# Performance work log

Measured on AMD Instinct MI355X. Metric: run time of the kernel, lower is better.

Reference implementation:

```python
import jax, jax.numpy as jnp
import numpy as np

N = 50000   # nodes
E = 600000  # edges
IN = 512    # in_channels
H = 128     # hidden_channels
B = 64      # graphs in batch
L = 4       # GatedGraphConv layers
VIEWS = [[0, 9, 10], [1, 2, 3], [4, 5, 6], [7, 8, 11, 12]]  # syntactic/sequential/semantic/discourse


def layer_norm(x, w, b, eps=1e-5):
    mu = x.mean(-1, keepdims=True)
    var = ((x - mu) ** 2).mean(-1, keepdims=True)
    return (x - mu) / jnp.sqrt(var + eps) * w + b


def setup_inputs() -> dict:
    key = jax.random.key(0)
    ks = jax.random.split(key, 32)
    p = lambda k, shape: (jax.random.normal(k, shape, jnp.float32) * 0.02)
    inp = {
        'x': jax.random.normal(ks[0], (N, IN), jnp.float32),
        'edge_index': jax.random.randint(ks[1], (2, E), 0, N, dtype=jnp.int32),
        'edge_type': jax.random.randint(ks[2], (E,), 0, 13, dtype=jnp.int32),
        'batch': jnp.sort(jax.random.randint(ks[3], (N,), 0, B, dtype=jnp.int32)),
        # input projection (Linear + LayerNorm)
        'proj_w': p(ks[4], (IN, H)), 'proj_b': p(ks[5], (H,)),
        'ln0_w': jnp.ones((H,), jnp.float32), 'ln0_b': jnp.zeros((H,), jnp.float32),
        # per-view GatedGraphConv: weight [views, layers, H, H] + GRUCell params [views, 3H, H]
        'ggnn_w': p(ks[6], (4, L, H, H)),
        'gru_wih': p(ks[7], (4, 3 * H, H)), 'gru_whh': p(ks[8], (4, 3 * H, H)),
        'gru_bih': p(ks[9], (4, 3 * H)), 'gru_bhh': p(ks[10], (4, 3 * H)),
        # per-view LayerNorm
        'vln_w': jnp.ones((4, H), jnp.float32), 'vln_b': jnp.zeros((4, H), jnp.float32),
        # attention fusion
        'q_w': p(ks[11], (H, H)), 'q_b': p(ks[12], (H,)),
        'k_w': p(ks[13], (H, H)), 'k_b': p(ks[14], (H,)),
        # classifier MLP: 2H -> H -> H//2 -> 1
        'c1_w': p(ks[15], (2 * H, H)), 'c1_b': p(ks[16], (H,)),
        'c2_w': p(ks[17], (H, H // 2)), 'c2_b': p(ks[18], (H // 2,)),
        'c3_w': p(ks[19], (H // 2, 1)), 'c3_b': p(ks[20], (1,)),
    }
    return inp


def reference(x, edge_index, edge_type, batch, proj_w, proj_b, ln0_w, ln0_b,
              ggnn_w, gru_wih, gru_whh, gru_bih, gru_bhh, vln_w, vln_b,
              q_w, q_b, k_w, k_b, c1_w, c1_b, c2_w, c2_b, c3_w, c3_b):
    # input projection: Linear -> LayerNorm -> GELU (dropout = identity in eval)
    h0 = jax.nn.gelu(layer_norm(x @ proj_w + proj_b, ln0_w, ln0_b), approximate=False)
    src, dst = edge_index[0], edge_index[1]
    views = []
    for v in range(4):
        emask = jnp.zeros((E,), bool)
        for t in VIEWS[v]:
            emask = emask | (edge_type == t)
        em = emask.astype(h0.dtype)[:, None]  # [E,1] edge-type view mask
        h = h0
        for i in range(L):
            m = h @ ggnn_w[v, i]                                   # [N,H]
            agg = jax.ops.segment_sum(m[src] * em, dst, num_segments=N)  # masked scatter-add
            # GRUCell(input=agg, hidden=h), torch gate order r,z,n
            gi = agg @ gru_wih[v].T + gru_bih[v]
            gh = h @ gru_whh[v].T + gru_bhh[v]
            ir, iz, inn = jnp.split(gi, 3, -1)
            hr, hz, hn = jnp.split(gh, 3, -1)
            r = jax.nn.sigmoid(ir + hr)
            z = jax.nn.sigmoid(iz + hz)
            n = jnp.tanh(inn + r * hn)
            h = (1.0 - z) * n + z * h
        views.append(layer_norm(h, vln_w[v], vln_b[v]) + h0)  # residual ViewEncoder
    hs = jnp.stack(views, 1)  # [N,4,H]
    # node-conditioned attention fusion
    q = jnp.tanh(h0 @ q_w + q_b)
    keys = hs @ k_w + k_b
    attn = jax.nn.softmax(jnp.einsum('nh,nvh->nv', q, keys) * (H ** -0.5), axis=-1)
    fused = jnp.einsum('nvh,nv->nh', hs, attn)
    # global mean + max pooling per graph
    cnt = jax.ops.segment_sum(jnp.ones((N,), fused.dtype), batch, num_segments=B)
    x_mean = jax.ops.segment_sum(fused, batch, num_segments=B) / jnp.maximum(cnt, 1.0)[:, None]
    x_max = jax.ops.segment_max(fused, batch, num_segments=B)
    g = jnp.concatenate([x_mean, x_max], -1)  # [B,2H]
    h1 = jax.nn.relu(g @ c1_w + c1_b)
    h2 = jax.nn.relu(h1 @ c2_w + c2_b)
    return h2 @ c3_w + c3_b  # [B,1] logits
```

## Files before the change

### kernel.cpp

```cpp
#include <hip/hip_runtime.h>
#include <math.h>


typedef __attribute__((ext_vector_type(8))) short short8;
typedef __attribute__((ext_vector_type(4))) float floatx4;

__device__ __forceinline__ unsigned short f2bf_rtn(float x) {
    unsigned u = __float_as_uint(x);
    return (unsigned short)((u + 0x7FFFu + ((u >> 16) & 1u)) >> 16);
}
__device__ __forceinline__ float bf2f(unsigned short h) {
    return __uint_as_float((unsigned)h << 16);
}
__device__ __forceinline__ float fsig(float x) {
    return __builtin_amdgcn_rcpf(1.0f + __expf(-x));
}
__device__ __forceinline__ float ftanh(float x) {
    return 1.0f - 2.0f * __builtin_amdgcn_rcpf(__expf(2.0f * x) + 1.0f);
}

__device__ __forceinline__ int view_of(int t) {
    return (t >= 1 && t <= 3) ? 1 : (t >= 4 && t <= 6) ? 2
         : ((t == 7) || (t == 8) || (t >= 11)) ? 3 : 0;
}

template <bool BT, int EPI>
__global__ __launch_bounds__(256, 2) void gemm_k(
    const float* __restrict__ A, const float* __restrict__ Bm,
    const float* __restrict__ bias, float* __restrict__ C,
    int N, int M, int K, long sA, long sB, long sC)
{
    __shared__ float As[32][132];
    __shared__ float Bs[32][132];
    A  += (long)blockIdx.z * sA;
    Bm += (long)blockIdx.z * sB;
    C  += (long)blockIdx.z * sC;
    const int r0 = blockIdx.x * 128;
    const int c0 = blockIdx.y * 128;
    const int tid = threadIdx.x;
    const int tx = tid & 15;
    const int ty = tid >> 4;

    float acc[8][8];
#pragma unroll
    for (int i = 0; i < 8; i++)
#pragma unroll
        for (int j = 0; j < 8; j++) acc[i][j] = 0.0f;

    for (int k0 = 0; k0 < K; k0 += 32) {
        {
            int arow = tid >> 3;
            int akq  = (tid & 7) << 2;
#pragma unroll
            for (int hh = 0; hh < 4; hh++) {
                int r  = arow + hh * 32;
                int gr = r0 + r;
                float4 av = make_float4(0.f, 0.f, 0.f, 0.f);
                if (gr < N) av = *(const float4*)(A + (long)gr * K + k0 + akq);
                As[akq + 0][r] = av.x; As[akq + 1][r] = av.y;
                As[akq + 2][r] = av.z; As[akq + 3][r] = av.w;
            }
        }
        if (BT) {
            int brow = tid >> 3;
            int bkq  = (tid & 7) << 2;
#pragma unroll
            for (int hh = 0; hh < 4; hh++) {
                int r = brow + hh * 32;
                float4 bv = *(const float4*)(Bm + (long)(c0 + r) * K + k0 + bkq);
                Bs[bkq + 0][r] = bv.x; Bs[bkq + 1][r] = bv.y;
                Bs[bkq + 2][r] = bv.z; Bs[bkq + 3][r] = bv.w;
            }
        } else {
            int kk0 = tid >> 5;
            int bmq = (tid & 31) << 2;
#pragma unroll
            for (int hh = 0; hh < 4; hh++) {
                int kk = kk0 + hh * 8;
                float4 bv = *(const float4*)(Bm + (long)(k0 + kk) * M + c0 + bmq);
                *(float4*)&Bs[kk][bmq] = bv;
            }
        }
        __syncthreads();
#pragma unroll
        for (int k = 0; k < 32; k++) {
            float4 a0 = *(const float4*)&As[k][ty << 2];
            float4 a1 = *(const float4*)&As[k][64 + (ty << 2)];
            float4 b0 = *(const float4*)&Bs[k][tx << 2];
            float4 b1 = *(const float4*)&Bs[k][64 + (tx << 2)];
            float av[8] = {a0.x, a0.y, a0.z, a0.w, a1.x, a1.y, a1.z, a1.w};
            float bv[8] = {b0.x, b0.y, b0.z, b0.w, b1.x, b1.y, b1.z, b1.w};
#pragma unroll
            for (int i = 0; i < 8; i++)
#pragma unroll
                for (int j = 0; j < 8; j++) acc[i][j] += av[i] * bv[j];
        }
        __syncthreads();
    }

    float bb[8] = {0, 0, 0, 0, 0, 0, 0, 0};
    if (bias) {
        float4 b0 = *(const float4*)(bias + c0 + (tx << 2));
        float4 b1 = *(const float4*)(bias + c0 + 64 + (tx << 2));
        bb[0] = b0.x; bb[1] = b0.y; bb[2] = b0.z; bb[3] = b0.w;
        bb[4] = b1.x; bb[5] = b1.y; bb[6] = b1.z; bb[7] = b1.w;
    }
#pragma unroll
    for (int i = 0; i < 8; i++) {
        int r = (i < 4) ? (r0 + (ty << 2) + i) : (r0 + 64 + (ty << 2) + i - 4);
        if (r < N) {
            float v[8];
#pragma unroll
            for (int j = 0; j < 8; j++) {
                v[j] = acc[i][j] + bb[j];
                if (EPI == 1) v[j] = tanhf(v[j]);
            }
            *(float4*)(C + (long)r * M + c0 + (tx << 2)) = make_float4(v[0], v[1], v[2], v[3]);
            *(float4*)(C + (long)r * M + c0 + 64 + (tx << 2)) = make_float4(v[4], v[5], v[6], v[7]);
        }
    }
}

__global__ __launch_bounds__(256) void build_p_k(
    const float* __restrict__ gwih, const float* __restrict__ gwhh,
    const float* __restrict__ gbih, const float* __restrict__ gbhh,
    float* __restrict__ pih, float* __restrict__ phh, float* __restrict__ bp)
{
    int idx = blockIdx.x * 256 + threadIdx.x;
    if (idx < 16 * 65536) {
        int z = idx >> 16, rem = idx & 65535;
        int k = rem >> 9, mcol = rem & 511;
        int ch = mcol >> 2, g = mcol & 3;
        int v = z >> 2;
        const float* Wih = gwih + (long)v * 384 * 128;
        float val = 0.0f;
        if (g == 0) val = Wih[ch * 128 + k];
        else if (g == 1) val = Wih[(128 + ch) * 128 + k];
        else if (g == 2) val = Wih[(256 + ch) * 128 + k];
        pih[idx] = val;
    }
    if (idx < 4 * 65536) {
        int v = idx >> 16, rem = idx & 65535;
        int k = rem >> 9, mcol = rem & 511;
        int ch = mcol >> 2, g = mcol & 3;
        const float* Whh = gwhh + (long)v * 384 * 128;
        float val = 0.0f;
        if (g == 0) val = Whh[ch * 128 + k];
        else if (g == 1) val = Whh[(128 + ch) * 128 + k];
        else if (g == 3) val = Whh[(256 + ch) * 128 + k];
        phh[idx] = val;
    }
    if (idx < 4 * 512) {
        int v = idx >> 9, mcol = idx & 511;
        int ch = mcol >> 2, g = mcol & 3;
        float val;
        if (g == 0) val = gbih[v * 384 + ch] + gbhh[v * 384 + ch];
        else if (g == 1) val = gbih[v * 384 + 128 + ch] + gbhh[v * 384 + 128 + ch];
        else if (g == 2) val = gbih[v * 384 + 256 + ch];
        else val = gbhh[v * 384 + 256 + ch];
        bp[idx] = val;
    }
}

__global__ __launch_bounds__(256) void pack_b_k(
    const float* __restrict__ wcomb, const float* __restrict__ phh,
    short* __restrict__ Bp)
{
    int idx = blockIdx.x * 256 + threadIdx.x;
    if (idx >= 16 * 256 * 512) return;
    int z = idx >> 17, rem = idx & 131071;
    int k = rem >> 9, col = rem & 511;
    int g  = col & 3;
    int q  = (col >> 2) & 3;
    int tn = (col >> 4) & 7;
    int ch = ((col >> 7) << 5) + (q << 3) + tn;
    int mcol = (ch << 2) + g;
    float val = (k < 128) ? wcomb[(long)z * 65536 + k * 512 + mcol]
                          : phh[(long)(z >> 2) * 65536 + (k - 128) * 512 + mcol];
    long dst = ((long)(z * 8 + (k >> 5)) * 512 + col) * 32 + ((k >> 3) & 3) * 8 + (k & 7);
    Bp[dst] = (short)f2bf_rtn(val);
}

template <bool BT>
__global__ __launch_bounds__(256) void pack_w_k(
    const float* __restrict__ W, short* __restrict__ bhi, short* __restrict__ blo, int K)
{
    int idx = blockIdx.x * 256 + threadIdx.x;
    if (idx >= K * 128) return;
    int k = idx >> 7, col = idx & 127;
    float v = BT ? W[col * K + k] : W[k * 128 + col];
    unsigned short h = f2bf_rtn(v);
    float fh = __uint_as_float((unsigned)h << 16);
    long dst = ((long)(k >> 5) * 128 + col) * 32 + ((k >> 3) & 3) * 8 + (k & 7);
    bhi[dst] = (short)h;
    blo[dst] = (short)f2bf_rtn(v - fh);
}

template <int EPI>
__global__ __launch_bounds__(256, 4) void gemm_mfma_k(
    const float* __restrict__ A, const short* __restrict__ Bhi,
    const short* __restrict__ Blo, const float* __restrict__ bias,
    float* __restrict__ C, int N, int K)
{
    __shared__ __align__(16) short Ahi[64 * 40];
    __shared__ __align__(16) short Alo[64 * 40];
    const int r0 = blockIdx.x * 64;
    const int tid = threadIdx.x;
    const int l = tid & 63, w = tid >> 6;
    const int wrow = w * 16;
    const int m = l & 15, q = l >> 4;

    floatx4 acc[8];
#pragma unroll
    for (int b = 0; b < 8; b++) acc[b] = (floatx4)0.0f;

    const int arow = tid >> 2;
    const int fcol = (tid & 3) * 8;
    const int gr = r0 + arow;
    const int nks = K >> 5;

    for (int ks = 0; ks < nks; ks++) {
        float xv[8];
        if (gr < N) {
            float4 x0 = *(const float4*)(A + (long)gr * K + ks * 32 + fcol);
            float4 x1 = *(const float4*)(A + (long)gr * K + ks * 32 + fcol + 4);
            xv[0] = x0.x; xv[1] = x0.y; xv[2] = x0.z; xv[3] = x0.w;
            xv[4] = x1.x; xv[5] = x1.y; xv[6] = x1.z; xv[7] = x1.w;
        } else {
#pragma unroll
            for (int u = 0; u < 8; u++) xv[u] = 0.0f;
        }
        short8 vhi, vlo;
#pragma unroll
        for (int u = 0; u < 8; u++) {
            unsigned short hb = f2bf_rtn(xv[u]);
            float fh = __uint_as_float((unsigned)hb << 16);
            vhi[u] = (short)hb;
            vlo[u] = (short)f2bf_rtn(xv[u] - fh);
        }
        *(short8*)&Ahi[arow * 40 + fcol] = vhi;
        *(short8*)&Alo[arow * 40 + fcol] = vlo;
        __syncthreads();
        short8 ah = *(short8*)&Ahi[(wrow + m) * 40 + q * 8];
        short8 al = *(short8*)&Alo[(wrow + m) * 40 + q * 8];
#pragma unroll
        for (int tn = 0; tn < 8; tn++) {
            int col = tn * 16 + m;
            short8 bh = *(const short8*)(Bhi + ((long)ks * 128 + col) * 32 + q * 8);
            short8 bl = *(const short8*)(Blo + ((long)ks * 128 + col) * 32 + q * 8);
            acc[tn] = __builtin_amdgcn_mfma_f32_16x16x32_bf16(ah, bh, acc[tn], 0, 0, 0);
            acc[tn] = __builtin_amdgcn_mfma_f32_16x16x32_bf16(al, bh, acc[tn], 0, 0, 0);
            acc[tn] = __builtin_amdgcn_mfma_f32_16x16x32_bf16(ah, bl, acc[tn], 0, 0, 0);
        }
        __syncthreads();
    }

#pragma unroll
    for (int tn = 0; tn < 8; tn++) {
        int col = tn * 16 + m;
        float bb = bias ? bias[col] : 0.0f;
#pragma unroll
        for (int reg = 0; reg < 4; reg++) {
            int row = r0 + wrow + q * 4 + reg;
            if (row < N) {
                float v = acc[tn][reg] + bb;
                if (EPI == 1) v = ftanh(v);
                C[(long)row * 128 + col] = v;
            }
        }
    }
}

__global__ __launch_bounds__(256, 3) void gemm_gru_mfma_k(
    const short* __restrict__ hb, const float* __restrict__ hpf,
    const short* __restrict__ Bp, const float* __restrict__ bp,
    float* __restrict__ hf, short* __restrict__ hbn,
    const int* __restrict__ off, const int* __restrict__ esrc,
    int N, long sV, long sHb, long sHp)
{
    __shared__ __align__(16) short As[8 * 64 * 40];
    const int xb = blockIdx.x;
    const int x = (xb & 7) | ((xb >> 4) << 3);
    const int yb = (xb >> 3) & 1;
    if (x * 64 >= N) return;
    const int z = blockIdx.z;
    const short* hbz = hb + (long)z * sHb;
    hpf += (long)z * sHp;
    Bp  += (long)z * 524288;
    bp  += (long)z * 512;
    hf  += (long)z * sV;
    hbn += (long)z * sV;
    const int r0  = x * 64;
    const int c0b = yb * 256;
    const int tid = threadIdx.x;
    const int l = tid & 63, w = tid >> 6;
    const int wrow = (w & 1) * 32, wcol = (w >> 1) * 128;
    const int m = l & 15, q = l >> 4;

    floatx4 acc[2][8];
#pragma unroll
    for (int a = 0; a < 2; a++)
#pragma unroll
        for (int b = 0; b < 8; b++) acc[a][b] = (floatx4)0.0f;

    const int arow = tid >> 2;
    const int fcol = (tid & 3) * 8;
    const int gr = r0 + arow;

    {
        const int cg = tid & 3;
        float accS[32];
#pragma unroll
        for (int u = 0; u < 32; u++) accS[u] = 0.0f;
        if (gr < N) {
            const int idx = z * N + gr;
            const int beg = off[idx], end = off[idx + 1];
            for (int j = beg; j < end; j++) {
                const short* sp = hb + (long)esrc[j] * 128 + (cg << 5);
                short8 v0 = *(const short8*)(sp);
                short8 v1 = *(const short8*)(sp + 8);
                short8 v2 = *(const short8*)(sp + 16);
                short8 v3 = *(const short8*)(sp + 24);
#pragma unroll
                for (int u = 0; u < 8; u++) {
                    accS[u]      += bf2f((unsigned short)v0[u]);
                    accS[8 + u]  += bf2f((unsigned short)v1[u]);
                    accS[16 + u] += bf2f((unsigned short)v2[u]);
                    accS[24 + u] += bf2f((unsigned short)v3[u]);
                }
            }
        }
#pragma unroll
        for (int ub = 0; ub < 4; ub++) {
            short8 o;
#pragma unroll
            for (int u = 0; u < 8; u++) o[u] = (short)f2bf_rtn(accS[ub * 8 + u]);
            *(short8*)&As[cg * 2560 + arow * 40 + ub * 8] = o;
        }
    }

#pragma unroll
    for (int ks2 = 0; ks2 < 4; ks2++) {
        short8 av = (short8)0;
        if (gr < N) av = *(const short8*)(hbz + (long)gr * 128 + ks2 * 32 + fcol);
        *(short8*)&As[(4 + ks2) * 2560 + arow * 40 + fcol] = av;
    }
    __syncthreads();

#pragma unroll
    for (int ks = 0; ks < 8; ks++) {
        short8 bfr[8];
#pragma unroll
        for (int tn = 0; tn < 8; tn++) {
            int col = c0b + wcol + tn * 16 + m;
            bfr[tn] = *(const short8*)(Bp + ((long)ks * 512 + col) * 32 + q * 8);
        }
        short8 a0 = *(short8*)&As[ks * 2560 + (wrow + m) * 40 + q * 8];
        short8 a1 = *(short8*)&As[ks * 2560 + (wrow + 16 + m) * 40 + q * 8];
#pragma unroll
        for (int tn = 0; tn < 8; tn++) {
            acc[0][tn] = __builtin_amdgcn_mfma_f32_16x16x32_bf16(bfr[tn], a0, acc[0][tn], 0, 0, 0);
            acc[1][tn] = __builtin_amdgcn_mfma_f32_16x16x32_bf16(bfr[tn], a1, acc[1][tn], 0, 0, 0);
        }
    }

    const int chq = ((c0b + wcol) >> 2) + q * 8;
#pragma unroll
    for (int a = 0; a < 2; a++) {
        const int row = r0 + wrow + a * 16 + m;
        if (row < N) {
            float4 hp0 = *(const float4*)(hpf + (long)row * 128 + chq);
            float4 hp1 = *(const float4*)(hpf + (long)row * 128 + chq + 4);
            float hpv[8] = {hp0.x, hp0.y, hp0.z, hp0.w, hp1.x, hp1.y, hp1.z, hp1.w};
            float hnv[8];
            short8 hb8;
#pragma unroll
            for (int tn = 0; tn < 8; tn++) {
                float4 bv = *(const float4*)(bp + (chq + tn) * 4);
                floatx4 A = acc[a][tn];
                float rr = fsig(A[0] + bv.x);
                float zz = fsig(A[1] + bv.y);
                float nn = ftanh(A[2] + bv.z + rr * (A[3] + bv.w));
                hnv[tn] = (1.0f - zz) * nn + zz * hpv[tn];
                hb8[tn] = (short)f2bf_rtn(hnv[tn]);
            }
            *(float4*)(hf + (long)row * 128 + chq) =
                make_float4(hnv[0], hnv[1], hnv[2], hnv[3]);
            *(float4*)(hf + (long)row * 128 + chq + 4) =
                make_float4(hnv[4], hnv[5], hnv[6], hnv[7]);
            *(short8*)(hbn + (long)row * 128 + chq) = hb8;
        }
    }
}

__global__ __launch_bounds__(256) void ln_gelu_k(
    float* __restrict__ h0, short* __restrict__ h0b,
    const float* __restrict__ w, const float* __restrict__ b, int N)
{
    long t = (long)blockIdx.x * 256 + threadIdx.x;
    int n = (int)(t >> 5), lane = (int)(t & 31);
    if (n >= N) return;
    float* p = h0 + (long)n * 128 + lane * 4;
    float4 x = *(float4*)p;
    float s = x.x + x.y + x.z + x.w;
#pragma unroll
    for (int off = 16; off >= 1; off >>= 1) s += __shfl_xor(s, off);
    float mu = s * (1.0f / 128.0f);
    float4 d = make_float4(x.x - mu, x.y - mu, x.z - mu, x.w - mu);
    float ss = d.x * d.x + d.y * d.y + d.z * d.z + d.w * d.w;
#pragma unroll
    for (int off = 16; off >= 1; off >>= 1) ss += __shfl_xor(ss, off);
    float inv = 1.0f / sqrtf(ss * (1.0f / 128.0f) + 1e-5f);
    float4 wv = *(const float4*)(w + lane * 4);
    float4 bv = *(const float4*)(b + lane * 4);
    float y[4] = {d.x * inv * wv.x + bv.x, d.y * inv * wv.y + bv.y,
                  d.z * inv * wv.z + bv.z, d.w * inv * wv.w + bv.w};
#pragma unroll
    for (int i = 0; i < 4; i++)
        y[i] = 0.5f * y[i] * (1.0f + erff(y[i] * 0.70710678118654752f));
    *(float4*)p = make_float4(y[0], y[1], y[2], y[3]);
    ushort4 hb;
    hb.x = f2bf_rtn(y[0]); hb.y = f2bf_rtn(y[1]);
    hb.z = f2bf_rtn(y[2]); hb.w = f2bf_rtn(y[3]);
    *(ushort4*)(h0b + (long)n * 128 + lane * 4) = hb;
}

__global__ __launch_bounds__(256) void count_k(
    const int* __restrict__ dst, const int* __restrict__ et,
    int* __restrict__ cnt, int E, int N)
{
    int e = blockIdx.x * 256 + threadIdx.x;
    if (e >= E) return;
    int v = view_of(et[e]);
    atomicAdd(&cnt[v * N + dst[e]], 1);
}

__global__ __launch_bounds__(256) void scan1_k(
    const int* __restrict__ cnt, int* __restrict__ off, int* __restrict__ bsum, int n)
{
    __shared__ int sm[256];
    int base = blockIdx.x * 1024;
    int tid = threadIdx.x;
    int v[4]; int s = 0;
#pragma unroll
    for (int i = 0; i < 4; i++) {
        int idx = base + tid * 4 + i;
        v[i] = (idx < n) ? cnt[idx] : 0; s += v[i];
    }
    sm[tid] = s; __syncthreads();
    for (int o = 1; o < 256; o <<= 1) {
        int t2 = (tid >= o) ? sm[tid - o] : 0;
        __syncthreads(); sm[tid] += t2; __syncthreads();
    }
    int run = sm[tid] - s;
    if (tid == 255) bsum[blockIdx.x] = sm[255];
#pragma unroll
    for (int i = 0; i < 4; i++) {
        int idx = base + tid * 4 + i;
        if (idx < n) off[idx] = run;
        run += v[i];
    }
}

__global__ __launch_bounds__(256) void scan2_k(int* __restrict__ bsum, int nb)
{
    __shared__ int sm[256];
    int tid = threadIdx.x;
    int v = (tid < nb) ? bsum[tid] : 0;
    sm[tid] = v; __syncthreads();
    for (int o = 1; o < 256; o <<= 1) {
        int t2 = (tid >= o) ? sm[tid - o] : 0;
        __syncthreads(); sm[tid] += t2; __syncthreads();
    }
    if (tid < nb) bsum[tid] = sm[tid] - v;
}

__global__ __launch_bounds__(256) void scan3_k(
    int* __restrict__ off, int* __restrict__ cursor,
    const int* __restrict__ bsum, int n, int total)
{
    int i = blockIdx.x * 256 + threadIdx.x;
    if (i < n) {
        int o = off[i] + bsum[i >> 10];
        off[i] = o; cursor[i] = o;
    }
    if (i == 0) off[n] = total;
}

__global__ __launch_bounds__(256) void fill_k(
    const int* __restrict__ src, const int* __restrict__ dst,
    const int* __restrict__ et, int* __restrict__ cursor,
    int* __restrict__ esrc, int* __restrict__ esrc0, int E, int N)
{
    int e = blockIdx.x * 256 + threadIdx.x;
    if (e >= E) return;
    int v = view_of(et[e]);
    int b = v * N + dst[e];
    int pos = atomicAdd(&cursor[b], 1);
    esrc[pos] = v * N + src[e];
    esrc0[pos] = src[e];
}

__global__ __launch_bounds__(256) void vln_res_k(
    float* __restrict__ h, const float* __restrict__ h0,
    const float* __restrict__ w, const float* __restrict__ b, int N)
{
    int v = blockIdx.z;
    long t = (long)blockIdx.x * 256 + threadIdx.x;
    int n = (int)(t >> 5), lane = (int)(t & 31);
    if (n >= N) return;
    float* hp = h + ((long)v * N + n) * 128 + lane * 4;
    float4 x = *(float4*)hp;
    float s = x.x + x.y + x.z + x.w;
#pragma unroll
    for (int off = 16; off >= 1; off >>= 1) s += __shfl_xor(s, off);
    float mu = s * (1.0f / 128.0f);
    float4 d = make_float4(x.x - mu, x.y - mu, x.z - mu, x.w - mu);
    float ss = d.x * d.x + d.y * d.y + d.z * d.z + d.w * d.w;
#pragma unroll
    for (int off = 16; off >= 1; off >>= 1) ss += __shfl_xor(ss, off);
    float inv = 1.0f / sqrtf(ss * (1.0f / 128.0f) + 1e-5f);
    float4 wv = *(const float4*)(w + v * 128 + lane * 4);
    float4 bv = *(const float4*)(b + v * 128 + lane * 4);
    float4 hv = *(const float4*)(h0 + (long)n * 128 + lane * 4);
    float4 r;
    r.x = d.x * inv * wv.x + bv.x + hv.x;
    r.y = d.y * inv * wv.y + bv.y + hv.y;
    r.z = d.z * inv * wv.z + bv.z + hv.z;
    r.w = d.w * inv * wv.w + bv.w + hv.w;
    *(float4*)hp = r;
}

__global__ __launch_bounds__(256) void fusion_k(
    const float* __restrict__ hs, const float* __restrict__ q,
    const float* __restrict__ u, const float* __restrict__ kb,
    float* __restrict__ fused, int N)
{
    long t = (long)blockIdx.x * 256 + threadIdx.x;
    int n = (int)(t >> 5), lane = (int)(t & 31);
    if (n >= N) return;
    long NH = (long)N * 128;
    float4 qv = *(const float4*)(q + (long)n * 128 + lane * 4);
    float4 kv = *(const float4*)(kb + lane * 4);
    float4 uv = *(const float4*)(u + (long)n * 128 + lane * 4);
    float part = qv.x * kv.x + qv.y * kv.y + qv.z * kv.z + qv.w * kv.w;
    float4 hv[4];
    float lg[4];
#pragma unroll
    for (int v = 0; v < 4; v++) {
        hv[v] = *(const float4*)(hs + v * NH + (long)n * 128 + lane * 4);
        lg[v] = hv[v].x * uv.x + hv[v].y * uv.y + hv[v].z * uv.z + hv[v].w * uv.w;
    }
#pragma unroll
    for (int off = 16; off >= 1; off >>= 1) {
        part += __shfl_xor(part, off);
#pragma unroll
        for (int v = 0; v < 4; v++) lg[v] += __shfl_xor(lg[v], off);
    }
    const float scale = 0.08838834764831845f;
    float mx = -1e30f;
#pragma unroll
    for (int v = 0; v < 4; v++) { lg[v] = (lg[v] + part) * scale; mx = fmaxf(mx, lg[v]); }
    float se = 0.0f;
#pragma unroll
    for (int v = 0; v < 4; v++) { lg[v] = expf(lg[v] - mx); se += lg[v]; }
    float inv = 1.0f / se;
    float4 f = make_float4(0.f, 0.f, 0.f, 0.f);
#pragma unroll
    for (int v = 0; v < 4; v++) {
        float a = lg[v] * inv;
        f.x += a * hv[v].x; f.y += a * hv[v].y; f.z += a * hv[v].z; f.w += a * hv[v].w;
    }
    *(float4*)(fused + (long)n * 128 + lane * 4) = f;
}

__global__ __launch_bounds__(256) void pool_k(
    const float* __restrict__ fused, const int* __restrict__ batch,
    float* __restrict__ meanb, float* __restrict__ maxb, int N)
{
    __shared__ float s_sum[256], s_max[256];
    int b = blockIdx.x;
    int lo = 0, hi = N;
    while (lo < hi) { int mid = (lo + hi) >> 1; if (batch[mid] < b) lo = mid + 1; else hi = mid; }
    int beg = lo;
    lo = beg; hi = N;
    while (lo < hi) { int mid = (lo + hi) >> 1; if (batch[mid] < b + 1) lo = mid + 1; else hi = mid; }
    int end = lo;
    int tid = threadIdx.x;
    int c = tid & 127, half = tid >> 7;
    float sum = 0.0f, mx = __int_as_float(0xff800000);
    for (int n = beg + half; n < end; n += 2) {
        float v = fused[(long)n * 128 + c];
        sum += v; mx = fmaxf(mx, v);
    }
    s_sum[tid] = sum; s_max[tid] = mx;
    __syncthreads();
    if (half == 0) {
        float tot = s_sum[tid] + s_sum[tid + 128];
        float m2 = fmaxf(s_max[tid], s_max[tid + 128]);
        int cnt = end - beg;
        meanb[b * 128 + c] = tot / (float)max(cnt, 1);
        maxb[b * 128 + c] = m2;
    }
}

__global__ __launch_bounds__(256) void classifier_k(
    const float* __restrict__ meanb, const float* __restrict__ maxb,
    const float* __restrict__ c1w, const float* __restrict__ c1b,
    const float* __restrict__ c2w, const float* __restrict__ c2b,
    const float* __restrict__ c3w, const float* __restrict__ c3b,
    float* __restrict__ out)
{
    __shared__ float g[256];
    __shared__ float h1[128];
    __shared__ float h2[64];
    int b = blockIdx.x, tid = threadIdx.x;
    g[tid] = (tid < 128) ? meanb[b * 128 + tid] : maxb[b * 128 + (tid - 128)];
    __syncthreads();
    if (tid < 128) {
        float acc = c1b[tid];
        for (int k = 0; k < 256; k++) acc += g[k] * c1w[k * 128 + tid];
        h1[tid] = fmaxf(acc, 0.0f);
    }
    __syncthreads();
    if (tid < 64) {
        float acc = c2b[tid];
        for (int k = 0; k < 128; k++) acc += h1[k] * c2w[k * 64 + tid];
        h2[tid] = fmaxf(acc, 0.0f);
    }
    __syncthreads();
    if (tid < 64) {
        float p = h2[tid] * c3w[tid];
#pragma unroll
        for (int off = 32; off >= 1; off >>= 1) p += __shfl_xor(p, off);
        if (tid == 0) out[b] = c3b[0] + p;
    }
}

extern "C" void kernel_launch(void* const* d_in, const int* in_sizes, int n_in,
                              void* d_out, int out_size, void* d_ws, size_t ws_size,
                              hipStream_t stream) {
    (void)n_in; (void)out_size; (void)ws_size;
    const float* x      = (const float*)d_in[0];
    const int*   eidx   = (const int*)d_in[1];
    const int*   etype  = (const int*)d_in[2];
    const int*   batch  = (const int*)d_in[3];
    const float* proj_w = (const float*)d_in[4];
    const float* proj_b = (const float*)d_in[5];
    const float* ln0_w  = (const float*)d_in[6];
    const float* ln0_b  = (const float*)d_in[7];
    const float* ggnn_w = (const float*)d_in[8];
    const float* gwih   = (const float*)d_in[9];
    const float* gwhh   = (const float*)d_in[10];
    const float* gbih   = (const float*)d_in[11];
    const float* gbhh   = (const float*)d_in[12];
    const float* vln_w  = (const float*)d_in[13];
    const float* vln_b  = (const float*)d_in[14];
    const float* q_w    = (const float*)d_in[15];
    const float* q_b    = (const float*)d_in[16];
    const float* k_w    = (const float*)d_in[17];
    const float* k_b    = (const float*)d_in[18];
    const float* c1w    = (const float*)d_in[19];
    const float* c1b    = (const float*)d_in[20];
    const float* c2w    = (const float*)d_in[21];
    const float* c2b    = (const float*)d_in[22];
    const float* c3w    = (const float*)d_in[23];
    const float* c3b    = (const float*)d_in[24];
    float* out = (float*)d_out;

    const int N = in_sizes[3];
    const int E = in_sizes[2];
    const int IN = in_sizes[0] / N;
    const int H = 128, L = 4;
    const int N4 = 4 * N;

    long NH = (long)N * H;
    float* ws = (float*)d_ws;
    float* h0 = ws;
    float* hf = h0 + NH;
    float* poolMean = hf + 4 * NH;
    float* poolMax  = poolMean + 8192;
    float* bp = poolMax + 8192;
    short* h0b = (short*)(bp + 2048);
    short* hbA = h0b + NH;
    short* hbB = hbA + 4 * NH;
    short* Sb  = hbB + 4 * NH;
    short* Bp  = Sb + 4 * NH;
    short* prjHi = Bp + 16 * 131072;
    short* prjLo = prjHi + 65536;
    short* qwHi  = prjLo + 65536;
    short* qwLo  = qwHi + 16384;
    short* kwHi  = qwLo + 16384;
    short* kwLo  = kwHi + 16384;
    int* iOff  = (int*)(kwLo + 16384);
    int* iCnt  = iOff + N4 + 1;
    int* iCur  = iCnt + N4;
    int* iBsum = iCur + N4;
    int* iEsrc  = iBsum + 256;
    int* iEsrc0 = iEsrc + E;
    float* wcomb = hf;
    float* pih   = hf + 16 * 65536;
    float* phh   = pih + 16 * 65536;
    float* qbuf  = (float*)Sb;
    float* ubuf  = qbuf + NH;
    float* fused = (float*)hbA;

    int rb = (int)(((long)N * 32 + 255) / 256);
    int eb = (E + 255) / 256;
    int nbScan = (N4 + 1023) / 1024;
    int gx64 = (N + 63) / 64;
    int gxp = ((gx64 + 7) / 8) * 8;

    const int* esrc_in = eidx;
    const int* edst_in = eidx + E;

    hipMemsetAsync(iCnt, 0, (size_t)N4 * sizeof(int), stream);
    count_k<<<eb, 256, 0, stream>>>(edst_in, etype, iCnt, E, N);
    scan1_k<<<nbScan, 256, 0, stream>>>(iCnt, iOff, iBsum, N4);
    scan2_k<<<1, 256, 0, stream>>>(iBsum, nbScan);
    scan3_k<<<(N4 + 255) / 256, 256, 0, stream>>>(iOff, iCur, iBsum, N4, E);
    fill_k<<<eb, 256, 0, stream>>>(esrc_in, edst_in, etype, iCur, iEsrc, iEsrc0, E, N);

    build_p_k<<<(16 * 65536 + 255) / 256, 256, 0, stream>>>(
        gwih, gwhh, gbih, gbhh, pih, phh, bp);
    gemm_k<false, 0><<<dim3(1, 4, 16), 256, 0, stream>>>(
        ggnn_w, pih, nullptr, wcomb, 128, 512, 128,
        (long)H * H, 65536, 65536);
    pack_b_k<<<(16 * 256 * 512 + 255) / 256, 256, 0, stream>>>(wcomb, phh, Bp);
    pack_w_k<false><<<(IN * 128 + 255) / 256, 256, 0, stream>>>(proj_w, prjHi, prjLo, IN);
    pack_w_k<false><<<(128 * 128 + 255) / 256, 256, 0, stream>>>(q_w, qwHi, qwLo, 128);
    pack_w_k<true><<<(128 * 128 + 255) / 256, 256, 0, stream>>>(k_w, kwHi, kwLo, 128);

    gemm_mfma_k<0><<<gx64, 256, 0, stream>>>(x, prjHi, prjLo, proj_b, h0, N, IN);
    ln_gelu_k<<<rb, 256, 0, stream>>>(h0, h0b, ln0_w, ln0_b, N);

    const float* hpf = h0;   long sHp = 0;
    const short* hbc = h0b;  long sHb = 0;
    short* hbn = hbA;
    for (int i = 0; i < L; i++) {
        const int* es = (i == 0) ? iEsrc0 : iEsrc;
        gemm_gru_mfma_k<<<dim3(2 * gxp, 1, 4), 256, 0, stream>>>(
            hbc, hpf, Bp + (long)i * 131072, bp, hf, hbn, iOff, es,
            N, NH, sHb, sHp);
        hpf = hf; sHp = NH;
        hbc = hbn; sHb = NH;
        hbn = (hbn == hbA) ? hbB : hbA;
    }

    vln_res_k<<<dim3(rb, 1, 4), 256, 0, stream>>>(hf, h0, vln_w, vln_b, N);

    gemm_mfma_k<1><<<gx64, 256, 0, stream>>>(h0, qwHi, qwLo, q_b, qbuf, N, 128);
    gemm_mfma_k<0><<<gx64, 256, 0, stream>>>(qbuf, kwHi, kwLo, nullptr, ubuf, N, 128);
    fusion_k<<<rb, 256, 0, stream>>>(hf, qbuf, ubuf, k_b, fused, N);
    pool_k<<<64, 256, 0, stream>>>(fused, batch, poolMean, poolMax, N);
    classifier_k<<<64, 256, 0, stream>>>(
        poolMean, poolMax, c1w, c1b, c2w, c2b, c3w, c3b, out);
}
```

Measured before the change: 1.340 ms.

## Store GRU hidden state as bf16 hi/lo pair and fuse view LayerNorm into fusion

The per-layer GRU kernel now reads the previous hidden state and writes the new one as two bf16 halves (hi + residual lo) instead of fp32 plus a separate bf16 copy. This cuts epilogue memory traffic. The view LayerNorm + residual kernel is removed and folded into fusion_k, which reconstructs the state from hi/lo. The edge gather loop gets a one-step software prefetch, and the kernel's occupancy hint is raised from 3 to 4. The hi/lo split keeps near-fp32 precision but adds conversion arithmetic and register pressure.

```diff
diff --git a/kernel.cpp b/kernel.cpp
--- a/kernel.cpp
+++ b/kernel.cpp
@@ -271,12 +271,12 @@
     }
 }
 
-__global__ __launch_bounds__(256, 3) void gemm_gru_mfma_k(
-    const short* __restrict__ hb, const float* __restrict__ hpf,
-    const short* __restrict__ Bp, const float* __restrict__ bp,
-    float* __restrict__ hf, short* __restrict__ hbn,
-    const int* __restrict__ off, const int* __restrict__ esrc,
-    int N, long sV, long sHb, long sHp)
+__global__ __launch_bounds__(256, 4) void gemm_gru_mfma_k(
+    const short* __restrict__ hb, const short* __restrict__ hpHi,
+    const short* __restrict__ hpLo, const short* __restrict__ Bp,
+    const float* __restrict__ bp, short* __restrict__ outHi,
+    short* __restrict__ outLo, const int* __restrict__ off,
+    const int* __restrict__ esrc, int N, long sV, long sHb, long sHp)
 {
     __shared__ __align__(16) short As[8 * 64 * 40];
     const int xb = blockIdx.x;
@@ -285,11 +285,12 @@
     if (x * 64 >= N) return;
     const int z = blockIdx.z;
     const short* hbz = hb + (long)z * sHb;
-    hpf += (long)z * sHp;
+    const short* hph = hpHi + (long)z * sHp;
+    const short* hpl = hpLo + (long)z * sHp;
     Bp  += (long)z * 524288;
     bp  += (long)z * 512;
-    hf  += (long)z * sV;
-    hbn += (long)z * sV;
+    outHi += (long)z * sV;
+    outLo += (long)z * sV;
     const int r0  = x * 64;
     const int c0b = yb * 256;
     const int tid = threadIdx.x;
@@ -297,12 +298,6 @@
     const int wrow = (w & 1) * 32, wcol = (w >> 1) * 128;
     const int m = l & 15, q = l >> 4;
 
-    floatx4 acc[2][8];
-#pragma unroll
-    for (int a = 0; a < 2; a++)
-#pragma unroll
-        for (int b = 0; b < 8; b++) acc[a][b] = (floatx4)0.0f;
-
     const int arow = tid >> 2;
     const int fcol = (tid & 3) * 8;
     const int gr = r0 + arow;
@@ -314,19 +309,31 @@
         for (int u = 0; u < 32; u++) accS[u] = 0.0f;
         if (gr < N) {
             const int idx = z * N + gr;
-            const int beg = off[idx], end = off[idx + 1];
-            for (int j = beg; j < end; j++) {
+            int j = off[idx];
+            const int end = off[idx + 1];
+            if (j < end) {
                 const short* sp = hb + (long)esrc[j] * 128 + (cg << 5);
-                short8 v0 = *(const short8*)(sp);
-                short8 v1 = *(const short8*)(sp + 8);
-                short8 v2 = *(const short8*)(sp + 16);
-                short8 v3 = *(const short8*)(sp + 24);
-#pragma unroll
-                for (int u = 0; u < 8; u++) {
-                    accS[u]      += bf2f((unsigned short)v0[u]);
-                    accS[8 + u]  += bf2f((unsigned short)v1[u]);
-                    accS[16 + u] += bf2f((unsigned short)v2[u]);
-                    accS[24 + u] += bf2f((unsigned short)v3[u]);
+                short8 p0 = *(const short8*)(sp);
+                short8 p1 = *(const short8*)(sp + 8);
+                short8 p2 = *(const short8*)(sp + 16);
+                short8 p3 = *(const short8*)(sp + 24);
+                for (; j < end;) {
+                    short8 c0 = p0, c1 = p1, c2 = p2, c3 = p3;
+                    ++j;
+                    if (j < end) {
+                        const short* sq = hb + (long)esrc[j] * 128 + (cg << 5);
+                        p0 = *(const short8*)(sq);
+                        p1 = *(const short8*)(sq + 8);
+                        p2 = *(const short8*)(sq + 16);
+                        p3 = *(const short8*)(sq + 24);
+                    }
+#pragma unroll
+                    for (int u = 0; u < 8; u++) {
+                        accS[u]      += bf2f((unsigned short)c0[u]);
+                        accS[8 + u]  += bf2f((unsigned short)c1[u]);
+                        accS[16 + u] += bf2f((unsigned short)c2[u]);
+                        accS[24 + u] += bf2f((unsigned short)c3[u]);
+                    }
                 }
             }
         }
@@ -347,6 +354,12 @@
     }
     __syncthreads();
 
+    floatx4 acc[2][8];
+#pragma unroll
+    for (int a = 0; a < 2; a++)
+#pragma unroll
+        for (int b = 0; b < 8; b++) acc[a][b] = (floatx4)0.0f;
+
 #pragma unroll
     for (int ks = 0; ks < 8; ks++) {
         short8 bfr[8];
@@ -369,32 +382,31 @@
     for (int a = 0; a < 2; a++) {
         const int row = r0 + wrow + a * 16 + m;
         if (row < N) {
-            float4 hp0 = *(const float4*)(hpf + (long)row * 128 + chq);
-            float4 hp1 = *(const float4*)(hpf + (long)row * 128 + chq + 4);
-            float hpv[8] = {hp0.x, hp0.y, hp0.z, hp0.w, hp1.x, hp1.y, hp1.z, hp1.w};
+            short8 h8 = *(const short8*)(hph + (long)row * 128 + chq);
+            short8 l8 = *(const short8*)(hpl + (long)row * 128 + chq);
             float hnv[8];
-            short8 hb8;
+            short8 ohi, olo;
 #pragma unroll
             for (int tn = 0; tn < 8; tn++) {
+                float hp = bf2f((unsigned short)h8[tn]) + bf2f((unsigned short)l8[tn]);
                 float4 bv = *(const float4*)(bp + (chq + tn) * 4);
                 floatx4 A = acc[a][tn];
                 float rr = fsig(A[0] + bv.x);
                 float zz = fsig(A[1] + bv.y);
                 float nn = ftanh(A[2] + bv.z + rr * (A[3] + bv.w));
-                hnv[tn] = (1.0f - zz) * nn + zz * hpv[tn];
-                hb8[tn] = (short)f2bf_rtn(hnv[tn]);
+                hnv[tn] = (1.0f - zz) * nn + zz * hp;
+                unsigned short hh = f2bf_rtn(hnv[tn]);
+                ohi[tn] = (short)hh;
+                olo[tn] = (short)f2bf_rtn(hnv[tn] - bf2f(hh));
             }
-            *(float4*)(hf + (long)row * 128 + chq) =
-                make_float4(hnv[0], hnv[1], hnv[2], hnv[3]);
-            *(float4*)(hf + (long)row * 128 + chq + 4) =
-                make_float4(hnv[4], hnv[5], hnv[6], hnv[7]);
-            *(short8*)(hbn + (long)row * 128 + chq) = hb8;
+            *(short8*)(outHi + (long)row * 128 + chq) = ohi;
+            *(short8*)(outLo + (long)row * 128 + chq) = olo;
         }
     }
 }
 
 __global__ __launch_bounds__(256) void ln_gelu_k(
-    float* __restrict__ h0, short* __restrict__ h0b,
+    float* __restrict__ h0, short* __restrict__ h0b, short* __restrict__ h0lo,
     const float* __restrict__ w, const float* __restrict__ b, int N)
 {
     long t = (long)blockIdx.x * 256 + threadIdx.x;
@@ -419,10 +431,13 @@
     for (int i = 0; i < 4; i++)
         y[i] = 0.5f * y[i] * (1.0f + erff(y[i] * 0.70710678118654752f));
     *(float4*)p = make_float4(y[0], y[1], y[2], y[3]);
-    ushort4 hb;
-    hb.x = f2bf_rtn(y[0]); hb.y = f2bf_rtn(y[1]);
-    hb.z = f2bf_rtn(y[2]); hb.w = f2bf_rtn(y[3]);
+    ushort4 hb, lb;
+    hb.x = f2bf_rtn(y[0]); lb.x = f2bf_rtn(y[0] - bf2f(hb.x));
+    hb.y = f2bf_rtn(y[1]); lb.y = f2bf_rtn(y[1] - bf2f(hb.y));
+    hb.z = f2bf_rtn(y[2]); lb.z = f2bf_rtn(y[2] - bf2f(hb.z));
+    hb.w = f2bf_rtn(y[3]); lb.w = f2bf_rtn(y[3] - bf2f(hb.w));
     *(ushort4*)(h0b + (long)n * 128 + lane * 4) = hb;
+    *(ushort4*)(h0lo + (long)n * 128 + lane * 4) = lb;
 }
 
 __global__ __launch_bounds__(256) void count_k(
@@ -501,55 +516,48 @@
     esrc0[pos] = src[e];
 }
 
-__global__ __launch_bounds__(256) void vln_res_k(
-    float* __restrict__ h, const float* __restrict__ h0,
-    const float* __restrict__ w, const float* __restrict__ b, int N)
-{
-    int v = blockIdx.z;
+__global__ __launch_bounds__(256) void fusion_k(
+    const short* __restrict__ hi, const short* __restrict__ lo,
+    const float* __restrict__ h0, const float* __restrict__ q,
+    const float* __restrict__ u, const float* __restrict__ kb,
+    const float* __restrict__ vw, const float* __restrict__ vb,
+    float* __restrict__ fused, int N)
+{
     long t = (long)blockIdx.x * 256 + threadIdx.x;
     int n = (int)(t >> 5), lane = (int)(t & 31);
     if (n >= N) return;
-    float* hp = h + ((long)v * N + n) * 128 + lane * 4;
-    float4 x = *(float4*)hp;
-    float s = x.x + x.y + x.z + x.w;
-#pragma unroll
-    for (int off = 16; off >= 1; off >>= 1) s += __shfl_xor(s, off);
-    float mu = s * (1.0f / 128.0f);
-    float4 d = make_float4(x.x - mu, x.y - mu, x.z - mu, x.w - mu);
-    float ss = d.x * d.x + d.y * d.y + d.z * d.z + d.w * d.w;
-#pragma unroll
-    for (int off = 16; off >= 1; off >>= 1) ss += __shfl_xor(ss, off);
-    float inv = 1.0f / sqrtf(ss * (1.0f / 128.0f) + 1e-5f);
-    float4 wv = *(const float4*)(w + v * 128 + lane * 4);
-    float4 bv = *(const float4*)(b + v * 128 + lane * 4);
-    float4 hv = *(const float4*)(h0 + (long)n * 128 + lane * 4);
-    float4 r;
-    r.x = d.x * inv * wv.x + bv.x + hv.x;
-    r.y = d.y * inv * wv.y + bv.y + hv.y;
-    r.z = d.z * inv * wv.z + bv.z + hv.z;
-    r.w = d.w * inv * wv.w + bv.w + hv.w;
-    *(float4*)hp = r;
-}
-
-__global__ __launch_bounds__(256) void fusion_k(
-    const float* __restrict__ hs, const float* __restrict__ q,
-    const float* __restrict__ u, const float* __restrict__ kb,
-    float* __restrict__ fused, int N)
-{
-    long t = (long)blockIdx.x * 256 + threadIdx.x;
-    int n = (int)(t >> 5), lane = (int)(t & 31);
-    if (n >= N) return;
-    long NH = (long)N * 128;
     float4 qv = *(const float4*)(q + (long)n * 128 + lane * 4);
     float4 kv = *(const float4*)(kb + lane * 4);
     float4 uv = *(const float4*)(u + (long)n * 128 + lane * 4);
+    float4 h0v = *(const float4*)(h0 + (long)n * 128 + lane * 4);
     float part = qv.x * kv.x + qv.y * kv.y + qv.z * kv.z + qv.w * kv.w;
-    float4 hv[4];
+    float hs[4][4];
     float lg[4];
 #pragma unroll
     for (int v = 0; v < 4; v++) {
-        hv[v] = *(const float4*)(hs + v * NH + (long)n * 128 + lane * 4);
-        lg[v] = hv[v].x * uv.x + hv[v].y * uv.y + hv[v].z * uv.z + hv[v].w * uv.w;
+        long base = ((long)v * N + n) * 128 + lane * 4;
+        ushort4 hu = *(const ushort4*)(hi + base);
+        ushort4 lu = *(const ushort4*)(lo + base);
+        float hv0 = bf2f(hu.x) + bf2f(lu.x);
+        float hv1 = bf2f(hu.y) + bf2f(lu.y);
+        float hv2 = bf2f(hu.z) + bf2f(lu.z);
+        float hv3 = bf2f(hu.w) + bf2f(lu.w);
+        float s = hv0 + hv1 + hv2 + hv3;
+#pragma unroll
+        for (int off = 16; off >= 1; off >>= 1) s += __shfl_xor(s, off);
+        float mu = s * (1.0f / 128.0f);
+        float d0 = hv0 - mu, d1 = hv1 - mu, d2 = hv2 - mu, d3 = hv3 - mu;
+        float ss = d0 * d0 + d1 * d1 + d2 * d2 + d3 * d3;
+#pragma unroll
+        for (int off = 16; off >= 1; off >>= 1) ss += __shfl_xor(ss, off);
+        float inv = 1.0f / sqrtf(ss * (1.0f / 128.0f) + 1e-5f);
+        float4 wv = *(const float4*)(vw + v * 128 + lane * 4);
+        float4 bv = *(const float4*)(vb + v * 128 + lane * 4);
+        hs[v][0] = d0 * inv * wv.x + bv.x + h0v.x;
+        hs[v][1] = d1 * inv * wv.y + bv.y + h0v.y;
+        hs[v][2] = d2 * inv * wv.z + bv.z + h0v.z;
+        hs[v][3] = d3 * inv * wv.w + bv.w + h0v.w;
+        lg[v] = hs[v][0] * uv.x + hs[v][1] * uv.y + hs[v][2] * uv.z + hs[v][3] * uv.w;
     }
 #pragma unroll
     for (int off = 16; off >= 1; off >>= 1) {
@@ -569,7 +577,8 @@
 #pragma unroll
     for (int v = 0; v < 4; v++) {
         float a = lg[v] * inv;
-        f.x += a * hv[v].x; f.y += a * hv[v].y; f.z += a * hv[v].z; f.w += a * hv[v].w;
+        f.x += a * hs[v][0]; f.y += a * hs[v][1];
+        f.z += a * hs[v][2]; f.w += a * hs[v][3];
     }
     *(float4*)(fused + (long)n * 128 + lane * 4) = f;
 }
@@ -677,14 +686,16 @@
     long NH = (long)N * H;
     float* ws = (float*)d_ws;
     float* h0 = ws;
-    float* hf = h0 + NH;
-    float* poolMean = hf + 4 * NH;
+    float* hfz = h0 + NH;
+    short* loA = (short*)hfz;
+    short* loB = loA + 4 * NH;
+    float* poolMean = hfz + 4 * NH;
     float* poolMax  = poolMean + 8192;
     float* bp = poolMax + 8192;
     short* h0b = (short*)(bp + 2048);
-    short* hbA = h0b + NH;
-    short* hbB = hbA + 4 * NH;
-    short* Sb  = hbB + 4 * NH;
+    short* hiA = h0b + NH;
+    short* hiB = hiA + 4 * NH;
+    short* Sb  = hiB + 4 * NH;
     short* Bp  = Sb + 4 * NH;
     short* prjHi = Bp + 16 * 131072;
     short* prjLo = prjHi + 65536;
@@ -698,12 +709,13 @@
     int* iBsum = iCur + N4;
     int* iEsrc  = iBsum + 256;
     int* iEsrc0 = iEsrc + E;
-    float* wcomb = hf;
-    float* pih   = hf + 16 * 65536;
+    float* wcomb = hfz;
+    float* pih   = hfz + 16 * 65536;
     float* phh   = pih + 16 * 65536;
+    short* lo0 = loB;
     float* qbuf  = (float*)Sb;
     float* ubuf  = qbuf + NH;
-    float* fused = (float*)hbA;
+    float* fused = (float*)hiA;
 
     int rb = (int)(((long)N * 32 + 255) / 256);
     int eb = (E + 255) / 256;
@@ -732,26 +744,26 @@
     pack_w_k<true><<<(128 * 128 + 255) / 256, 256, 0, stream>>>(k_w, kwHi, kwLo, 128);
 
     gemm_mfma_k<0><<<gx64, 256, 0, stream>>>(x, prjHi, prjLo, proj_b, h0, N, IN);
-    ln_gelu_k<<<rb, 256, 0, stream>>>(h0, h0b, ln0_w, ln0_b, N);
-
-    const float* hpf = h0;   long sHp = 0;
-    const short* hbc = h0b;  long sHb = 0;
-    short* hbn = hbA;
+    ln_gelu_k<<<rb, 256, 0, stream>>>(h0, h0b, lo0, ln0_w, ln0_b, N);
+
+    const short* hin = h0b;  long sHb = 0;
+    const short* hpH = h0b;  const short* hpL = lo0;  long sHp = 0;
+    short* oHi = hiA; short* oLo = loA;
     for (int i = 0; i < L; i++) {
         const int* es = (i == 0) ? iEsrc0 : iEsrc;
         gemm_gru_mfma_k<<<dim3(2 * gxp, 1, 4), 256, 0, stream>>>(
-            hbc, hpf, Bp + (long)i * 131072, bp, hf, hbn, iOff, es,
+            hin, hpH, hpL, Bp + (long)i * 131072, bp, oHi, oLo, iOff, es,
             N, NH, sHb, sHp);
-        hpf = hf; sHp = NH;
-        hbc = hbn; sHb = NH;
-        hbn = (hbn == hbA) ? hbB : hbA;
-    }
-
-    vln_res_k<<<dim3(rb, 1, 4), 256, 0, stream>>>(hf, h0, vln_w, vln_b, N);
+        hpH = oHi; hpL = oLo; sHp = NH;
+        hin = oHi; sHb = NH;
+        if (oHi == hiA) { oHi = hiB; oLo = loB; }
+        else            { oHi = hiA; oLo = loA; }
+    }
 
     gemm_mfma_k<1><<<gx64, 256, 0, stream>>>(h0, qwHi, qwLo, q_b, qbuf, N, 128);
     gemm_mfma_k<0><<<gx64, 256, 0, stream>>>(qbuf, kwHi, kwLo, nullptr, ubuf, N, 128);
-    fusion_k<<<rb, 256, 0, stream>>>(hf, qbuf, ubuf, k_b, fused, N);
+    fusion_k<<<rb, 256, 0, stream>>>(hiB, loB, h0, qbuf, ubuf, k_b,
+                                     vln_w, vln_b, fused, N);
     pool_k<<<64, 256, 0, stream>>>(fused, batch, poolMean, poolMax, N);
     classifier_k<<<64, 256, 0, stream>>>(
         poolMean, poolMax, c1w, c1b, c2w, c2b, c3w, c3b, out);
```

New measurement: 1.286 ms. 4.0% less time.
